# Performance work log

Measured on AMD Instinct MI355X. Metric: run time of the kernel, lower is better.

Reference implementation:

```python
import jax, jax.numpy as jnp
import numpy as np

N = 50000          # total nodes (1000 graphs x 50 agents)
E = 800000         # edges
B = 1000           # batch of graphs -> one agent node each
IN_DIM = 64
HID = 32           # hidden_dim == TransformerConv out_channels per head
HEADS = 4
OUT_DIM = 5
FINAL = HID + HID * HEADS * 2  # 288


def _tconv(x, src, dst, wq, bq, wk, bk, wv, bv):
    """PyG TransformerConv, root_weight=False, concat=True, no edge_attr."""
    n = x.shape[0]
    q = (x @ wq + bq).reshape(n, HEADS, HID)
    k = (x @ wk + bk).reshape(n, HEADS, HID)
    v = (x @ wv + bv).reshape(n, HEADS, HID)
    # per-edge attention logits: query at target, key at source
    alpha = jnp.sum(q[dst] * k[src], axis=-1) / jnp.sqrt(jnp.float32(HID))  # [E, HEADS]
    # segment softmax over incoming edges of each target node
    amax = jax.lax.stop_gradient(jax.ops.segment_max(alpha, dst, num_segments=n))
    ex = jnp.exp(alpha - amax[dst])
    denom = jax.ops.segment_sum(ex, dst, num_segments=n)
    attn = ex / (denom[dst] + 1e-16)                                        # [E, HEADS]
    out = jax.ops.segment_sum(v[src] * attn[..., None], dst, num_segments=n)
    return out.reshape(n, HEADS * HID)


def setup_inputs() -> dict:
    key = jax.random.key(0)
    ks = jax.random.split(key, 24)
    g = lambda i, shape, fan: (jax.random.normal(ks[i], shape, jnp.float32)
                               / jnp.sqrt(jnp.float32(fan)))
    d1 = HID * HEADS  # conv1 output width / conv2 input width
    inp = {
        "x": jax.random.normal(ks[0], (N, IN_DIM), jnp.float32),
        "edge_index": jax.random.randint(ks[1], (2, E), 0, N, jnp.int64),
        "dm_mask": (jax.random.uniform(ks[2], (N, 1)) > 0.5).astype(jnp.float32),
        "global_indices": jax.random.randint(ks[3], (B,), 0, N, jnp.int64),
        # encoder MLP: in -> hid (relu) -> hid
        "enc_w1": g(4, (IN_DIM, HID), IN_DIM), "enc_b1": jnp.zeros((HID,), jnp.float32),
        "enc_w2": g(5, (HID, HID), HID),       "enc_b2": jnp.zeros((HID,), jnp.float32),
        # conv1: hid -> heads*hid
        "c1_wq": g(6, (HID, d1), HID), "c1_bq": jnp.zeros((d1,), jnp.float32),
        "c1_wk": g(7, (HID, d1), HID), "c1_bk": jnp.zeros((d1,), jnp.float32),
        "c1_wv": g(8, (HID, d1), HID), "c1_bv": jnp.zeros((d1,), jnp.float32),
        # conv2: heads*hid -> heads*hid
        "c2_wq": g(9, (d1, d1), d1),  "c2_bq": jnp.zeros((d1,), jnp.float32),
        "c2_wk": g(10, (d1, d1), d1), "c2_bk": jnp.zeros((d1,), jnp.float32),
        "c2_wv": g(11, (d1, d1), d1), "c2_bv": jnp.zeros((d1,), jnp.float32),
        # output head
        "out_w": g(12, (FINAL, OUT_DIM), FINAL),
        "out_b": jnp.zeros((OUT_DIM,), jnp.float32),
    }
    return inp


def reference(x, edge_index, dm_mask, global_indices,
              enc_w1, enc_b1, enc_w2, enc_b2,
              c1_wq, c1_bq, c1_wk, c1_bk, c1_wv, c1_bv,
              c2_wq, c2_bq, c2_wk, c2_bk, c2_wv, c2_bv,
              out_w, out_b):
    src, dst = edge_index[0], edge_index[1]
    # encoder MLP + relu (forward applies F.relu on encoder output)
    h = jax.nn.relu(x @ enc_w1 + enc_b1)
    h = jax.nn.relu(h @ enc_w2 + enc_b2)            # [N, HID]
    x1 = h[global_indices]                          # [B, HID]
    h = jax.nn.relu(_tconv(h, src, dst, c1_wq, c1_bq, c1_wk, c1_bk, c1_wv, c1_bv))
    x2 = h[global_indices]                          # [B, HEADS*HID]
    h = h * dm_mask                                 # decision-maker masking
    h = jax.nn.relu(_tconv(h, src, dst, c2_wq, c2_bq, c2_wk, c2_bk, c2_wv, c2_bv))
    x3 = h[global_indices]                          # [B, HEADS*HID]
    x_cat = jnp.concatenate([x1, x2, x3], axis=1)   # [B, FINAL]
    return x_cat @ out_w + out_b                    # [B, OUT_DIM]
```

## Files before the change

kernel.cpp:

```cpp
#include <hip/hip_runtime.h>
#include <math.h>


typedef _Float16 half8 __attribute__((ext_vector_type(8)));
typedef float f32x4 __attribute__((ext_vector_type(4)));

__device__ inline half8 h8zero() {
    half8 r;
#pragma unroll
    for (int j = 0; j < 8; ++j) r[j] = (_Float16)0.f;
    return r;
}

__global__ __launch_bounds__(256)
void enc_kernel(const float* __restrict__ x,
                const float* __restrict__ w1, const float* __restrict__ b1,
                const float* __restrict__ w2, const float* __restrict__ b2,
                _Float16* __restrict__ h0, int n) {
    __shared__ float W1s[64 * 32];
    __shared__ float W2s[32 * 32];
    __shared__ float B1s[32], B2s[32];
    __shared__ float xs[8 * 64];
    __shared__ float hs[8 * 32];
    int t = threadIdx.x;
    for (int i = t; i < 64 * 32; i += 256) W1s[i] = w1[i];
    for (int i = t; i < 32 * 32; i += 256) W2s[i] = w2[i];
    if (t < 32) { B1s[t] = b1[t]; B2s[t] = b2[t]; }
    int bn = blockIdx.x * 8;
    if (t < 128) {
        int row = t >> 4;
        float4 val = make_float4(0.f, 0.f, 0.f, 0.f);
        if (bn + row < n) val = *(const float4*)(x + (size_t)bn * 64 + t * 4);
        ((float4*)xs)[t] = val;
    }
    __syncthreads();
    int nn = t >> 5, c = t & 31;
    float acc = B1s[c];
#pragma unroll
    for (int i = 0; i < 64; ++i) acc += xs[nn * 64 + i] * W1s[i * 32 + c];
    acc = fmaxf(acc, 0.f);
    hs[nn * 32 + c] = acc;
    __syncthreads();
    float acc2 = B2s[c];
#pragma unroll
    for (int i = 0; i < 32; ++i) acc2 += hs[nn * 32 + i] * W2s[i * 32 + c];
    acc2 = fmaxf(acc2, 0.f);
    int node = bn + nn;
    if (node < n) h0[(size_t)node * 32 + c] = (_Float16)acc2;
}

__global__ void wt_kernel(const float* __restrict__ q1, const float* __restrict__ k1,
                          const float* __restrict__ v1, _Float16* __restrict__ WT1,
                          const float* __restrict__ q2, const float* __restrict__ k2,
                          const float* __restrict__ v2, _Float16* __restrict__ WT2) {
    int tid = blockIdx.x * 256 + threadIdx.x;
    const int n1 = 3 * 128 * 32;
    const int n2 = 3 * 128 * 128;
    if (tid < n1) {
        int z = tid / (128 * 32);
        int rem = tid % (128 * 32);
        int c = rem / 32, k = rem % 32;
        const float* w = (z == 0) ? q1 : ((z == 1) ? k1 : v1);
        WT1[tid] = (_Float16)w[k * 128 + c];
    } else {
        int i = tid - n1;
        if (i >= n2) return;
        int z = i / (128 * 128);
        int rem = i % (128 * 128);
        int c = rem / 128, k = rem % 128;
        const float* w = (z == 0) ? q2 : ((z == 1) ? k2 : v2);
        WT2[i] = (_Float16)w[k * 128 + c];
    }
}

__global__ __launch_bounds__(256)
void qkv_kernel(const _Float16* __restrict__ X, const float* __restrict__ mask,
                const _Float16* __restrict__ WT,
                const float* __restrict__ Bq, const float* __restrict__ Bk,
                const float* __restrict__ Bv,
                _Float16* __restrict__ Q, _Float16* __restrict__ KV,
                int n, int IN) {
    __shared__ _Float16 Xs[64 * 40];
    __shared__ _Float16 Ws[128 * 40];
    int t = threadIdx.x;
    int z = blockIdx.y;
    int bm = blockIdx.x * 64;
    const float* Bz = (z == 0) ? Bq : ((z == 1) ? Bk : Bv);
    _Float16* Y;
    size_t ystride;
    if (z == 0) { Y = Q; ystride = 128; }
    else        { Y = KV + (z == 1 ? 0 : 128); ystride = 256; }

    int lane = t & 63, w = t >> 6;
    int wr = w >> 1, wc = w & 1;
    int fr = lane & 15, k0 = (lane >> 4) * 8;
    f32x4 acc[2][4];
#pragma unroll
    for (int i = 0; i < 2; ++i)
#pragma unroll
        for (int j = 0; j < 4; ++j)
#pragma unroll
            for (int r = 0; r < 4; ++r) acc[i][j][r] = 0.f;

    int srow = t >> 2, sseg = (t & 3) * 8;
    int snode = bm + srow;
    const _Float16* xbase = X + (size_t)snode * IN + sseg;
    const _Float16* wbase = WT + (size_t)(z * 128) * IN + sseg;
    bool xvalid = (snode < n);
    if (xvalid && mask) xvalid = (mask[snode] != 0.f);

    for (int kt = 0; kt < IN; kt += 32) {
        half8 xv = h8zero();
        if (xvalid) xv = *(const half8*)(xbase + kt);
        half8 wv0 = *(const half8*)(wbase + (size_t)srow * IN + kt);
        half8 wv1 = *(const half8*)(wbase + (size_t)(64 + srow) * IN + kt);
        __syncthreads();
        *(half8*)&Xs[srow * 40 + sseg] = xv;
        *(half8*)&Ws[srow * 40 + sseg] = wv0;
        *(half8*)&Ws[(64 + srow) * 40 + sseg] = wv1;
        __syncthreads();
        half8 a0 = *(const half8*)&Xs[(wr * 32 + fr) * 40 + k0];
        half8 a1 = *(const half8*)&Xs[(wr * 32 + 16 + fr) * 40 + k0];
#pragma unroll
        for (int tc = 0; tc < 4; ++tc) {
            half8 b = *(const half8*)&Ws[(wc * 64 + tc * 16 + fr) * 40 + k0];
            acc[0][tc] = __builtin_amdgcn_mfma_f32_16x16x32_f16(a0, b, acc[0][tc], 0, 0, 0);
            acc[1][tc] = __builtin_amdgcn_mfma_f32_16x16x32_f16(a1, b, acc[1][tc], 0, 0, 0);
        }
    }
#pragma unroll
    for (int tc = 0; tc < 4; ++tc) {
        int colc = wc * 64 + tc * 16 + fr;
        float bias = Bz[colc];
#pragma unroll
        for (int tr = 0; tr < 2; ++tr) {
#pragma unroll
            for (int reg = 0; reg < 4; ++reg) {
                int node = bm + wr * 32 + tr * 16 + (lane >> 4) * 4 + reg;
                if (node < n) Y[(size_t)node * ystride + colc] = (_Float16)(acc[tr][tc][reg] + bias);
            }
        }
    }
}

__global__ void hist_kernel(const int* __restrict__ dst, int* __restrict__ deg,
                            int* __restrict__ eslot, int e) {
    int i = blockIdx.x * 256 + threadIdx.x;
    if (i < e) eslot[i] = atomicAdd(&deg[dst[i]], 1);
}
__global__ void scan1_kernel(const int* __restrict__ deg, int* __restrict__ rp,
                             int* __restrict__ bsum, int n) {
    __shared__ int s[256];
    int t = threadIdx.x;
    int gid = blockIdx.x * 256 + t;
    int v = (gid < n) ? deg[gid] : 0;
    s[t] = v;
    __syncthreads();
#pragma unroll
    for (int off = 1; off < 256; off <<= 1) {
        int tv = (t >= off) ? s[t - off] : 0;
        __syncthreads();
        s[t] += tv;
        __syncthreads();
    }
    if (gid < n) rp[gid] = s[t] - v;
    if (t == 255) bsum[blockIdx.x] = s[255];
}
__global__ void scan2_kernel(int* bsum, int nb) {
    __shared__ int s[256];
    int t = threadIdx.x;
    int v = (t < nb) ? bsum[t] : 0;
    s[t] = v;
    __syncthreads();
#pragma unroll
    for (int off = 1; off < 256; off <<= 1) {
        int tv = (t >= off) ? s[t - off] : 0;
        __syncthreads();
        s[t] += tv;
        __syncthreads();
    }
    if (t < nb) bsum[t] = s[t] - v;
}
__global__ void scan3_kernel(int* rp, const int* __restrict__ bsum, int n) {
    int gid = blockIdx.x * 256 + threadIdx.x;
    if (gid < n) rp[gid] += bsum[blockIdx.x];
}
__global__ void scatter_kernel(const int* __restrict__ src, const int* __restrict__ dst,
                               const int* __restrict__ rp, const int* __restrict__ eslot,
                               int* __restrict__ col, int e) {
    int i = blockIdx.x * 256 + threadIdx.x;
    if (i < e) col[rp[dst[i]] + eslot[i]] = src[i];
}

__global__ __launch_bounds__(256)
void attn_kernel(const _Float16* __restrict__ q, const _Float16* __restrict__ kv,
                 const int* __restrict__ rp, const int* __restrict__ deg,
                 const int* __restrict__ col,
                 _Float16* __restrict__ out, int n) {
    int w = threadIdx.x >> 6;
    int lane = threadIdx.x & 63;
    int node = blockIdx.x * 4 + w;
    if (node >= n) return;
    int es = lane >> 4;
    int l = lane & 15;
    int d0 = l * 8;
    half8 qh = *(const half8*)(q + (size_t)node * 128 + d0);
    int start = rp[node], len = deg[node];
    float s = 0.f;
    float acc[8];
#pragma unroll
    for (int j = 0; j < 8; ++j) acc[j] = 0.f;
    const float sc = 0.17677669529663689f * 1.4426950408889634f;

    for (int i = es; i < len; i += 4) {
        int srcn = col[start + i];
        const _Float16* row = kv + (size_t)srcn * 256 + d0;
        half8 kf = *(const half8*)row;
        float dot = 0.f;
#pragma unroll
        for (int j = 0; j < 8; ++j) dot += (float)qh[j] * (float)kf[j];
        dot += __shfl_xor(dot, 1);
        dot += __shfl_xor(dot, 2);
        float a = fminf(fmaxf(dot * sc, -120.f), 120.f);
        float p = __builtin_amdgcn_exp2f(a);
        half8 vf = *(const half8*)(row + 128);
        s += p;
#pragma unroll
        for (int j = 0; j < 8; ++j) acc[j] += p * (float)vf[j];
    }
#pragma unroll
    for (int half = 16; half <= 32; half <<= 1) {
        s += __shfl_xor(s, half);
#pragma unroll
        for (int j = 0; j < 8; ++j) acc[j] += __shfl_xor(acc[j], half);
    }
    if (es == 0) {
        float inv = 1.f / (s + 1e-16f);
        half8 r;
#pragma unroll
        for (int j = 0; j < 8; ++j) r[j] = (_Float16)fmaxf(acc[j] * inv, 0.f);
        *(half8*)(out + (size_t)node * 128 + d0) = r;
    }
}

__global__ void head_kernel(const _Float16* __restrict__ h0, const _Float16* __restrict__ h1,
                            const _Float16* __restrict__ h2, const int* __restrict__ gi,
                            const float* __restrict__ ow, const float* __restrict__ ob,
                            float* __restrict__ out, int bsz) {
    int idx = blockIdx.x * 256 + threadIdx.x;
    if (idx >= bsz * 5) return;
    int b = idx / 5, c = idx % 5;
    int g = gi[b];
    float acc = ob[c];
    const _Float16* r0 = h0 + (size_t)g * 32;
#pragma unroll
    for (int i = 0; i < 32; ++i) acc += (float)r0[i] * ow[i * 5 + c];
    const _Float16* r1 = h1 + (size_t)g * 128;
#pragma unroll
    for (int i = 0; i < 128; ++i) acc += (float)r1[i] * ow[(32 + i) * 5 + c];
    const _Float16* r2 = h2 + (size_t)g * 128;
#pragma unroll
    for (int i = 0; i < 128; ++i) acc += (float)r2[i] * ow[(160 + i) * 5 + c];
    out[idx] = acc;
}

extern "C" void kernel_launch(void* const* d_in, const int* in_sizes, int n_in,
                              void* d_out, int out_size, void* d_ws, size_t ws_size,
                              hipStream_t stream) {
    const float* x    = (const float*)d_in[0];
    const int*   ei   = (const int*)d_in[1];
    const float* dm   = (const float*)d_in[2];
    const int*   gi   = (const int*)d_in[3];
    const float* ew1  = (const float*)d_in[4];
    const float* eb1  = (const float*)d_in[5];
    const float* ew2  = (const float*)d_in[6];
    const float* eb2  = (const float*)d_in[7];
    const float* c1wq = (const float*)d_in[8];
    const float* c1bq = (const float*)d_in[9];
    const float* c1wk = (const float*)d_in[10];
    const float* c1bk = (const float*)d_in[11];
    const float* c1wv = (const float*)d_in[12];
    const float* c1bv = (const float*)d_in[13];
    const float* c2wq = (const float*)d_in[14];
    const float* c2bq = (const float*)d_in[15];
    const float* c2wk = (const float*)d_in[16];
    const float* c2bk = (const float*)d_in[17];
    const float* c2wv = (const float*)d_in[18];
    const float* c2bv = (const float*)d_in[19];
    const float* ow   = (const float*)d_in[20];
    const float* ob   = (const float*)d_in[21];
    float* out = (float*)d_out;

    int N = in_sizes[0] / 64;
    int E = in_sizes[1] / 2;
    int B = in_sizes[3];
    const int* srcv = ei;
    const int* dstv = ei + E;

    char* ws = (char*)d_ws;
    size_t off = 0;
    auto alloc = [&](size_t bytes) -> void* {
        void* p = ws + off;
        off += (bytes + 255) & ~(size_t)255;
        return p;
    };
    _Float16* h0   = (_Float16*)alloc((size_t)N * 32 * 2);
    _Float16* h1   = (_Float16*)alloc((size_t)N * 128 * 2);
    _Float16* h2   = (_Float16*)alloc((size_t)N * 128 * 2);
    _Float16* Q    = (_Float16*)alloc((size_t)N * 128 * 2);
    _Float16* KV   = (_Float16*)alloc((size_t)N * 256 * 2);
    _Float16* WT1  = (_Float16*)alloc((size_t)3 * 128 * 32 * 2);
    _Float16* WT2  = (_Float16*)alloc((size_t)3 * 128 * 128 * 2);
    int* deg   = (int*)alloc((size_t)N * 4);
    int* rp    = (int*)alloc((size_t)N * 4);
    int* eslot = (int*)alloc((size_t)E * 4);
    int* colb  = (int*)alloc((size_t)E * 4);
    int* bsum  = (int*)alloc(4096);

    hipMemsetAsync(deg, 0, (size_t)N * 4, stream);

    int eb = (E + 255) / 256;
    int nb = (N + 255) / 256;
    wt_kernel<<<(3 * 128 * 32 + 3 * 128 * 128 + 255) / 256, 256, 0, stream>>>(
        c1wq, c1wk, c1wv, WT1, c2wq, c2wk, c2wv, WT2);
    hist_kernel<<<eb, 256, 0, stream>>>(dstv, deg, eslot, E);
    scan1_kernel<<<nb, 256, 0, stream>>>(deg, rp, bsum, N);
    scan2_kernel<<<1, 256, 0, stream>>>(bsum, nb);
    scan3_kernel<<<nb, 256, 0, stream>>>(rp, bsum, N);
    scatter_kernel<<<eb, 256, 0, stream>>>(srcv, dstv, rp, eslot, colb, E);

    enc_kernel<<<(N + 7) / 8, 256, 0, stream>>>(x, ew1, eb1, ew2, eb2, h0, N);

    dim3 gq((N + 63) / 64, 3);
    qkv_kernel<<<gq, 256, 0, stream>>>(h0, nullptr, WT1, c1bq, c1bk, c1bv, Q, KV, N, 32);
    attn_kernel<<<(N + 3) / 4, 256, 0, stream>>>(Q, KV, rp, deg, colb, h1, N);
    qkv_kernel<<<gq, 256, 0, stream>>>(h1, dm, WT2, c2bq, c2bk, c2bv, Q, KV, N, 128);
    attn_kernel<<<(N + 3) / 4, 256, 0, stream>>>(Q, KV, rp, deg, colb, h2, N);

    head_kernel<<<(B * 5 + 255) / 256, 256, 0, stream>>>(h0, h1, h2, gi, ow, ob, out, B);
}
```

Baseline: 252.9 us.

## Merge independent prep kernels into combined launches via block-index dispatch

Weight transpose, edge histogram and encoder MLP now run as one launch, with blockIdx ranges selecting the role. The block scan and the first QKV projection are merged the same way, since they are independent. This cuts kernel launches and lets unrelated work share the GPU at once. The attention kernel also converts the query to float once, outside the edge loop. In exchange, blocks of different roles share one shared-memory allocation and register budget, which may lower occupancy for the lighter roles.

```diff
diff --git a/kernel.cpp b/kernel.cpp
--- a/kernel.cpp
+++ b/kernel.cpp
@@ -12,21 +12,21 @@
     return r;
 }
 
-__global__ __launch_bounds__(256)
-void enc_kernel(const float* __restrict__ x,
-                const float* __restrict__ w1, const float* __restrict__ b1,
-                const float* __restrict__ w2, const float* __restrict__ b2,
-                _Float16* __restrict__ h0, int n) {
-    __shared__ float W1s[64 * 32];
-    __shared__ float W2s[32 * 32];
-    __shared__ float B1s[32], B2s[32];
-    __shared__ float xs[8 * 64];
-    __shared__ float hs[8 * 32];
+__device__ __forceinline__ void enc_body(const float* __restrict__ x,
+                                         const float* __restrict__ w1, const float* __restrict__ b1,
+                                         const float* __restrict__ w2, const float* __restrict__ b2,
+                                         _Float16* __restrict__ h0, int n, int bn,
+                                         float* __restrict__ smem) {
+    float* W1s = smem;
+    float* W2s = smem + 2048;
+    float* B1s = smem + 3072;
+    float* B2s = smem + 3104;
+    float* xs  = smem + 3136;
+    float* hs  = smem + 3648;
     int t = threadIdx.x;
     for (int i = t; i < 64 * 32; i += 256) W1s[i] = w1[i];
     for (int i = t; i < 32 * 32; i += 256) W2s[i] = w2[i];
     if (t < 32) { B1s[t] = b1[t]; B2s[t] = b2[t]; }
-    int bn = blockIdx.x * 8;
     if (t < 128) {
         int row = t >> 4;
         float4 val = make_float4(0.f, 0.f, 0.f, 0.f);
@@ -49,42 +49,55 @@
     if (node < n) h0[(size_t)node * 32 + c] = (_Float16)acc2;
 }
 
-__global__ void wt_kernel(const float* __restrict__ q1, const float* __restrict__ k1,
-                          const float* __restrict__ v1, _Float16* __restrict__ WT1,
-                          const float* __restrict__ q2, const float* __restrict__ k2,
-                          const float* __restrict__ v2, _Float16* __restrict__ WT2) {
-    int tid = blockIdx.x * 256 + threadIdx.x;
-    const int n1 = 3 * 128 * 32;
-    const int n2 = 3 * 128 * 128;
-    if (tid < n1) {
-        int z = tid / (128 * 32);
-        int rem = tid % (128 * 32);
-        int c = rem / 32, k = rem % 32;
-        const float* w = (z == 0) ? q1 : ((z == 1) ? k1 : v1);
-        WT1[tid] = (_Float16)w[k * 128 + c];
+__global__ __launch_bounds__(256)
+void prep_kernel(const float* __restrict__ x,
+                 const float* __restrict__ ew1, const float* __restrict__ eb1,
+                 const float* __restrict__ ew2, const float* __restrict__ eb2,
+                 _Float16* __restrict__ h0,
+                 const float* __restrict__ q1, const float* __restrict__ k1,
+                 const float* __restrict__ v1, _Float16* __restrict__ WT1,
+                 const float* __restrict__ q2, const float* __restrict__ k2,
+                 const float* __restrict__ v2, _Float16* __restrict__ WT2,
+                 const int* __restrict__ dstv, int* __restrict__ deg, int* __restrict__ eslot,
+                 int n, int e, int wtb, int histb) {
+    __shared__ float smem[3904];
+    int b = blockIdx.x, t = threadIdx.x;
+    if (b < wtb) {
+        int tid = b * 256 + t;
+        const int n1 = 3 * 128 * 32;
+        if (tid < n1) {
+            int z = tid / (128 * 32);
+            int rem = tid % (128 * 32);
+            int c = rem / 32, k = rem % 32;
+            const float* w = (z == 0) ? q1 : ((z == 1) ? k1 : v1);
+            WT1[tid] = (_Float16)w[k * 128 + c];
+        } else {
+            int i = tid - n1;
+            if (i < 3 * 128 * 128) {
+                int z = i / (128 * 128);
+                int rem = i % (128 * 128);
+                int c = rem / 128, k = rem % 128;
+                const float* w = (z == 0) ? q2 : ((z == 1) ? k2 : v2);
+                WT2[i] = (_Float16)w[k * 128 + c];
+            }
+        }
+    } else if (b < wtb + histb) {
+        int i = (b - wtb) * 256 + t;
+        if (i < e) eslot[i] = atomicAdd(&deg[dstv[i]], 1);
     } else {
-        int i = tid - n1;
-        if (i >= n2) return;
-        int z = i / (128 * 128);
-        int rem = i % (128 * 128);
-        int c = rem / 128, k = rem % 128;
-        const float* w = (z == 0) ? q2 : ((z == 1) ? k2 : v2);
-        WT2[i] = (_Float16)w[k * 128 + c];
-    }
-}
-
-__global__ __launch_bounds__(256)
-void qkv_kernel(const _Float16* __restrict__ X, const float* __restrict__ mask,
-                const _Float16* __restrict__ WT,
-                const float* __restrict__ Bq, const float* __restrict__ Bk,
-                const float* __restrict__ Bv,
-                _Float16* __restrict__ Q, _Float16* __restrict__ KV,
-                int n, int IN) {
-    __shared__ _Float16 Xs[64 * 40];
-    __shared__ _Float16 Ws[128 * 40];
+        enc_body(x, ew1, eb1, ew2, eb2, h0, n, (b - wtb - histb) * 8, smem);
+    }
+}
+
+__device__ __forceinline__ void qkv_body(const _Float16* __restrict__ X, const float* __restrict__ mask,
+                                         const _Float16* __restrict__ WT,
+                                         const float* __restrict__ Bq, const float* __restrict__ Bk,
+                                         const float* __restrict__ Bv,
+                                         _Float16* __restrict__ Q, _Float16* __restrict__ KV,
+                                         int n, int IN, int bx, int z,
+                                         _Float16* __restrict__ Xs, _Float16* __restrict__ Ws) {
     int t = threadIdx.x;
-    int z = blockIdx.y;
-    int bm = blockIdx.x * 64;
+    int bm = bx * 64;
     const float* Bz = (z == 0) ? Bq : ((z == 1) ? Bk : Bv);
     _Float16* Y;
     size_t ystride;
@@ -123,9 +136,9 @@
         half8 a1 = *(const half8*)&Xs[(wr * 32 + 16 + fr) * 40 + k0];
 #pragma unroll
         for (int tc = 0; tc < 4; ++tc) {
-            half8 b = *(const half8*)&Ws[(wc * 64 + tc * 16 + fr) * 40 + k0];
-            acc[0][tc] = __builtin_amdgcn_mfma_f32_16x16x32_f16(a0, b, acc[0][tc], 0, 0, 0);
-            acc[1][tc] = __builtin_amdgcn_mfma_f32_16x16x32_f16(a1, b, acc[1][tc], 0, 0, 0);
+            half8 bfr = *(const half8*)&Ws[(wc * 64 + tc * 16 + fr) * 40 + k0];
+            acc[0][tc] = __builtin_amdgcn_mfma_f32_16x16x32_f16(a0, bfr, acc[0][tc], 0, 0, 0);
+            acc[1][tc] = __builtin_amdgcn_mfma_f32_16x16x32_f16(a1, bfr, acc[1][tc], 0, 0, 0);
         }
     }
 #pragma unroll
@@ -143,29 +156,49 @@
     }
 }
 
-__global__ void hist_kernel(const int* __restrict__ dst, int* __restrict__ deg,
-                            int* __restrict__ eslot, int e) {
-    int i = blockIdx.x * 256 + threadIdx.x;
-    if (i < e) eslot[i] = atomicAdd(&deg[dst[i]], 1);
-}
-__global__ void scan1_kernel(const int* __restrict__ deg, int* __restrict__ rp,
-                             int* __restrict__ bsum, int n) {
-    __shared__ int s[256];
-    int t = threadIdx.x;
-    int gid = blockIdx.x * 256 + t;
-    int v = (gid < n) ? deg[gid] : 0;
-    s[t] = v;
-    __syncthreads();
-#pragma unroll
-    for (int off = 1; off < 256; off <<= 1) {
-        int tv = (t >= off) ? s[t - off] : 0;
-        __syncthreads();
-        s[t] += tv;
-        __syncthreads();
-    }
-    if (gid < n) rp[gid] = s[t] - v;
-    if (t == 255) bsum[blockIdx.x] = s[255];
-}
+__global__ __launch_bounds__(256)
+void scan1_qkv1_kernel(const int* __restrict__ deg, int* __restrict__ rp,
+                       int* __restrict__ bsum, int n, int nb,
+                       const _Float16* __restrict__ h0, const _Float16* __restrict__ WT1,
+                       const float* __restrict__ bq, const float* __restrict__ bk,
+                       const float* __restrict__ bv,
+                       _Float16* __restrict__ Q, _Float16* __restrict__ KV, int nqx) {
+    __shared__ _Float16 sm[64 * 40 + 128 * 40];
+    int b = blockIdx.x;
+    if (b < nb) {
+        int* s = (int*)sm;
+        int t = threadIdx.x;
+        int gid = b * 256 + t;
+        int v = (gid < n) ? deg[gid] : 0;
+        s[t] = v;
+        __syncthreads();
+#pragma unroll
+        for (int off = 1; off < 256; off <<= 1) {
+            int tv = (t >= off) ? s[t - off] : 0;
+            __syncthreads();
+            s[t] += tv;
+            __syncthreads();
+        }
+        if (gid < n) rp[gid] = s[t] - v;
+        if (t == 255) bsum[b] = s[255];
+    } else {
+        int r = b - nb;
+        int z = r / nqx, bx = r % nqx;
+        qkv_body(h0, nullptr, WT1, bq, bk, bv, Q, KV, n, 32, bx, z, sm, sm + 64 * 40);
+    }
+}
+
+__global__ __launch_bounds__(256)
+void qkv2_kernel(const _Float16* __restrict__ X, const float* __restrict__ mask,
+                 const _Float16* __restrict__ WT,
+                 const float* __restrict__ Bq, const float* __restrict__ Bk,
+                 const float* __restrict__ Bv,
+                 _Float16* __restrict__ Q, _Float16* __restrict__ KV, int n, int IN) {
+    __shared__ _Float16 Xs[64 * 40];
+    __shared__ _Float16 Ws[128 * 40];
+    qkv_body(X, mask, WT, Bq, Bk, Bv, Q, KV, n, IN, blockIdx.x, blockIdx.y, Xs, Ws);
+}
+
 __global__ void scan2_kernel(int* bsum, int nb) {
     __shared__ int s[256];
     int t = threadIdx.x;
@@ -204,7 +237,12 @@
     int es = lane >> 4;
     int l = lane & 15;
     int d0 = l * 8;
-    half8 qh = *(const half8*)(q + (size_t)node * 128 + d0);
+    float qf[8];
+    {
+        half8 qh = *(const half8*)(q + (size_t)node * 128 + d0);
+#pragma unroll
+        for (int j = 0; j < 8; ++j) qf[j] = (float)qh[j];
+    }
     int start = rp[node], len = deg[node];
     float s = 0.f;
     float acc[8];
@@ -218,7 +256,7 @@
         half8 kf = *(const half8*)row;
         float dot = 0.f;
 #pragma unroll
-        for (int j = 0; j < 8; ++j) dot += (float)qh[j] * (float)kf[j];
+        for (int j = 0; j < 8; ++j) dot += qf[j] * (float)kf[j];
         dot += __shfl_xor(dot, 1);
         dot += __shfl_xor(dot, 2);
         float a = fminf(fmaxf(dot * sc, -120.f), 120.f);
@@ -321,20 +359,25 @@
 
     int eb = (E + 255) / 256;
     int nb = (N + 255) / 256;
-    wt_kernel<<<(3 * 128 * 32 + 3 * 128 * 128 + 255) / 256, 256, 0, stream>>>(
-        c1wq, c1wk, c1wv, WT1, c2wq, c2wk, c2wv, WT2);
-    hist_kernel<<<eb, 256, 0, stream>>>(dstv, deg, eslot, E);
-    scan1_kernel<<<nb, 256, 0, stream>>>(deg, rp, bsum, N);
+    int nqx = (N + 63) / 64;
+    int wtb = (3 * 128 * 32 + 3 * 128 * 128 + 255) / 256;
+
+    prep_kernel<<<wtb + eb + (N + 7) / 8, 256, 0, stream>>>(
+        x, ew1, eb1, ew2, eb2, h0,
+        c1wq, c1wk, c1wv, WT1, c2wq, c2wk, c2wv, WT2,
+        dstv, deg, eslot, N, E, wtb, eb);
+
+    scan1_qkv1_kernel<<<nb + 3 * nqx, 256, 0, stream>>>(
+        deg, rp, bsum, N, nb, h0, WT1, c1bq, c1bk, c1bv, Q, KV, nqx);
+
     scan2_kernel<<<1, 256, 0, stream>>>(bsum, nb);
     scan3_kernel<<<nb, 256, 0, stream>>>(rp, bsum, N);
     scatter_kernel<<<eb, 256, 0, stream>>>(srcv, dstv, rp, eslot, colb, E);
 
-    enc_kernel<<<(N + 7) / 8, 256, 0, stream>>>(x, ew1, eb1, ew2, eb2, h0, N);
-
-    dim3 gq((N + 63) / 64, 3);
-    qkv_kernel<<<gq, 256, 0, stream>>>(h0, nullptr, WT1, c1bq, c1bk, c1bv, Q, KV, N, 32);
     attn_kernel<<<(N + 3) / 4, 256, 0, stream>>>(Q, KV, rp, deg, colb, h1, N);
-    qkv_kernel<<<gq, 256, 0, stream>>>(h1, dm, WT2, c2bq, c2bk, c2bv, Q, KV, N, 128);
+
+    dim3 gq(nqx, 3);
+    qkv2_kernel<<<gq, 256, 0, stream>>>(h1, dm, WT2, c2bq, c2bk, c2bv, Q, KV, N, 128);
     attn_kernel<<<(N + 3) / 4, 256, 0, stream>>>(Q, KV, rp, deg, colb, h2, N);
 
     head_kernel<<<(B * 5 + 255) / 256, 256, 0, stream>>>(h0, h1, h2, gi, ow, ob, out, B);
```

Result: faster. 244.9 us (-3.1%).
